# Kernel optimization log

Hardware: AMD Instinct MI355X
Metric: run time of the kernel (lower is better)

## Reference

```python
import jax, jax.numpy as jnp
import numpy as np

BUCKET_SIZE = 64  # must divide seq_len


def setup_inputs() -> dict:
    key = jax.random.key(0)
    k1, k2, k3, k4 = jax.random.split(key, 4)
    B, S, D = 4, 4096, 1024
    query = jax.random.normal(k1, (B, S, D), dtype=jnp.float32)
    key_t = jax.random.normal(k2, (B, S, D), dtype=jnp.float32)
    value = jax.random.normal(k3, (B, S, D), dtype=jnp.float32)
    # random hashing hyperplanes: [B, D, bucket_size // 2]
    R = jax.random.normal(k4, (B, D, BUCKET_SIZE // 2), dtype=jnp.float32)
    return {"query": query, "key": key_t, "value": value, "R": R}


def reference(query, key, value, R):
    B, S, D = query.shape
    # random projection: [B, S, bucket_size // 2]
    xR = jnp.einsum("bsd,bdr->bsr", query, R)
    # mirror trick -> [B, S, bucket_size]
    concat_xR = jnp.concatenate([xR, -xR], axis=-1)
    buckets = jnp.argmax(concat_xR, axis=-1)          # [B, S] int
    sticker = jnp.argsort(buckets, axis=-1)            # token permutation into buckets
    undo_sort = jnp.argsort(sticker, axis=-1)          # computed in original (unused)
    # batched gather (tf.gather batch_dims=1, axis=1)
    sorted_query = jnp.take_along_axis(query, sticker[..., None], axis=1)
    sorted_value = jnp.take_along_axis(value, sticker[..., None], axis=1)
    # tf.split(x, bucket_size, 1) then stack(axis=1) == reshape to chunks
    chunked_query = sorted_query.reshape(B, BUCKET_SIZE, S // BUCKET_SIZE, D)
    chunked_value = sorted_value.reshape(B, BUCKET_SIZE, S // BUCKET_SIZE, D)
    del undo_sort, chunked_query, chunked_value  # dead code in original; module returns sticker
    return sticker
```

## Files before the change

kernel.cpp:

```cpp
#include <hip/hip_runtime.h>


#define B_DIM 4
#define S_LEN 4096
#define D_DIM 1024
#define NR 32
#define NBK 64
#define TM 64
#define NCHUNK (S_LEN / TM)
#define NW 16
#define KSLICE (D_DIM / NW)

__global__ __launch_bounds__(1024, 4) void k1_buckets(
    const float* __restrict__ Q, const float* __restrict__ R,
    int* __restrict__ buckets, int* __restrict__ hist)
{
    __shared__ float buf[NW][NR][TM];
    __shared__ int cnt[NBK];

    const int t = threadIdx.x;
    const int b = blockIdx.x >> 6;
    const int chunk = blockIdx.x & 63;
    const int lane = t & 63;
    const int w = __builtin_amdgcn_readfirstlane(t >> 6);

    const int gtok = chunk * TM + lane;
    const float* Qrow = Q + ((size_t)b * S_LEN + gtok) * D_DIM + w * KSLICE;
    const float4* R4 = reinterpret_cast<const float4*>(
        R + (size_t)b * D_DIM * NR) + (size_t)w * KSLICE * (NR / 4);

    float4 acc[8];
#pragma unroll
    for (int rc = 0; rc < 8; ++rc) acc[rc] = make_float4(0.f, 0.f, 0.f, 0.f);

#pragma unroll
    for (int ph = 0; ph < 2; ++ph) {
        float4 qv[8];
#pragma unroll
        for (int j = 0; j < 8; ++j)
            qv[j] = *reinterpret_cast<const float4*>(Qrow + ph * 32 + j * 4);

#pragma unroll
        for (int kk = 0; kk < 32; ++kk) {
            const int k = ph * 32 + kk;
            const float4 qq = qv[kk >> 2];
            const float qk = ((kk & 3) == 0) ? qq.x
                           : ((kk & 3) == 1) ? qq.y
                           : ((kk & 3) == 2) ? qq.z : qq.w;
#pragma unroll
            for (int rc = 0; rc < 8; ++rc) {
                const float4 rv = R4[k * 8 + rc];
                acc[rc].x = fmaf(qk, rv.x, acc[rc].x);
                acc[rc].y = fmaf(qk, rv.y, acc[rc].y);
                acc[rc].z = fmaf(qk, rv.z, acc[rc].z);
                acc[rc].w = fmaf(qk, rv.w, acc[rc].w);
            }
        }
    }

#pragma unroll
    for (int rc = 0; rc < 8; ++rc) {
        buf[w][rc * 4 + 0][lane] = acc[rc].x;
        buf[w][rc * 4 + 1][lane] = acc[rc].y;
        buf[w][rc * 4 + 2][lane] = acc[rc].z;
        buf[w][rc * 4 + 3][lane] = acc[rc].w;
    }
    if (t < NBK) cnt[t] = 0;
    __syncthreads();

    if (t < TM) {
        float x[NR];
#pragma unroll
        for (int r = 0; r < NR; ++r) {
            float s = 0.f;
#pragma unroll
            for (int ww = 0; ww < NW; ++ww) s += buf[ww][r][t];
            x[r] = s;
        }
        float m1 = x[0]; int i1 = 0;
        float m2 = x[0]; int i2 = 0;
#pragma unroll
        for (int r = 1; r < NR; ++r) {
            const float v = x[r];
            if (v > m1) { m1 = v; i1 = r; }
            if (v < m2) { m2 = v; i2 = r; }
        }
        const int bk = (m1 >= -m2) ? i1 : (NR + i2);
        buckets[(size_t)b * S_LEN + chunk * TM + t] = bk;
        atomicAdd(&cnt[bk], 1);
    }
    __syncthreads();
    if (t < NBK) hist[((size_t)b * NCHUNK + chunk) * NBK + t] = cnt[t];
}

__global__ __launch_bounds__(256) void k2_scan(
    const int* __restrict__ hist, int* __restrict__ chunkOffset)
{
    const int t = threadIdx.x;
    const int b = t >> 6;
    const int bk = t & 63;
    const int lane = t & 63;

    int total = 0;
    for (int c = 0; c < NCHUNK; ++c)
        total += hist[((size_t)b * NCHUNK + c) * NBK + bk];

    int incl = total;
#pragma unroll
    for (int off = 1; off < 64; off <<= 1) {
        int n = __shfl_up(incl, off, 64);
        if (lane >= off) incl += n;
    }
    int run = incl - total;

    for (int c = 0; c < NCHUNK; ++c) {
        int h = hist[((size_t)b * NCHUNK + c) * NBK + bk];
        chunkOffset[((size_t)b * NCHUNK + c) * NBK + bk] = run;
        run += h;
    }
}

__global__ __launch_bounds__(256) void k3_scatter(
    const int* __restrict__ buckets, const int* __restrict__ chunkOffset,
    int* __restrict__ out)
{
    const int gid = blockIdx.x * 256 + threadIdx.x;
    const int b = gid >> 12;
    const int s = gid & (S_LEN - 1);
    const int chunk = s >> 6;
    const int lane = threadIdx.x & 63;

    const int bk = buckets[gid];

    unsigned long long m = ~0ull;
#pragma unroll
    for (int i = 0; i < 6; ++i) {
        unsigned long long bi = __ballot((bk >> i) & 1);
        m &= ((bk >> i) & 1) ? bi : ~bi;
    }
    int rank = __popcll(m & ((1ull << lane) - 1ull));

    int pos = chunkOffset[((size_t)b * NCHUNK + chunk) * NBK + bk] + rank;
    out[(size_t)b * S_LEN + pos] = s;
}

extern "C" void kernel_launch(void* const* d_in, const int* in_sizes, int n_in,
                              void* d_out, int out_size, void* d_ws, size_t ws_size,
                              hipStream_t stream) {
    const float* Q = (const float*)d_in[0];
    const float* R = (const float*)d_in[3];

    int* buckets     = (int*)d_ws;
    int* hist        = buckets + B_DIM * S_LEN;
    int* chunkOffset = hist + B_DIM * NCHUNK * NBK;

    k1_buckets<<<B_DIM * NCHUNK, 1024, 0, stream>>>(Q, R, buckets, hist);
    k2_scan   <<<1,              256,  0, stream>>>(hist, chunkOffset);
    k3_scatter<<<(B_DIM * S_LEN) / 256, 256, 0, stream>>>(buckets, chunkOffset, (int*)d_out);
}
```

Measured before the change: 46.17 us.

## Hold R slice in registers and stream Q tokens per wave with shuffle reduction

Rewrites the projection kernel so each lane keeps a 32-element column slice of R in registers. The wave then walks the 64 tokens of its chunk, loading each Q row segment as contiguous float4 vectors, double-buffered across token pairs. Partial dot products are combined with a cross-half shuffle and written to a padded shared buffer. The cross-wave reduction is now spread over all 1024 threads instead of 64. The aim is coalesced Q loads and the removal of repeated R global reads, at the cost of a serial per-token loop with more shared-memory stores and an extra barrier.

Measured after the change: 121.6 us. +163.3%, slower.

```diff
diff --git a/kernel.cpp b/kernel.cpp
--- a/kernel.cpp
+++ b/kernel.cpp
@@ -9,81 +9,90 @@
 #define TM 64
 #define NCHUNK (S_LEN / TM)
 #define NW 16
-#define KSLICE (D_DIM / NW)
+#define BUFP (NR + 1)
 
 __global__ __launch_bounds__(1024, 4) void k1_buckets(
     const float* __restrict__ Q, const float* __restrict__ R,
     int* __restrict__ buckets, int* __restrict__ hist)
 {
-    __shared__ float buf[NW][NR][TM];
+    __shared__ float buf[NW * TM * BUFP];
+    __shared__ float xs[NR * TM];
     __shared__ int cnt[NBK];
 
     const int t = threadIdx.x;
     const int b = blockIdx.x >> 6;
     const int chunk = blockIdx.x & 63;
+    const int w = t >> 6;
     const int lane = t & 63;
-    const int w = __builtin_amdgcn_readfirstlane(t >> 6);
+    const int r = lane & 31;
+    const int half = lane >> 5;
 
-    const int gtok = chunk * TM + lane;
-    const float* Qrow = Q + ((size_t)b * S_LEN + gtok) * D_DIM + w * KSLICE;
-    const float4* R4 = reinterpret_cast<const float4*>(
-        R + (size_t)b * D_DIM * NR) + (size_t)w * KSLICE * (NR / 4);
+    const float* Rb = R + (size_t)b * D_DIM * NR + (size_t)(w * 64 + half * 32) * NR + r;
+    float Rreg[32];
+#pragma unroll
+    for (int j = 0; j < 32; ++j) Rreg[j] = Rb[j * NR];
 
-    float4 acc[8];
+    const float* Qb = Q + ((size_t)b * S_LEN + chunk * TM) * D_DIM
+                    + w * 64 + half * 32;
+
+    float4 qA[8], qB[8];
 #pragma unroll
-    for (int rc = 0; rc < 8; ++rc) acc[rc] = make_float4(0.f, 0.f, 0.f, 0.f);
+    for (int i = 0; i < 8; ++i)
+        qA[i] = *reinterpret_cast<const float4*>(Qb + 0 * D_DIM + i * 4);
 
-#pragma unroll
-    for (int ph = 0; ph < 2; ++ph) {
-        float4 qv[8];
-#pragma unroll
-        for (int j = 0; j < 8; ++j)
-            qv[j] = *reinterpret_cast<const float4*>(Qrow + ph * 32 + j * 4);
-
-#pragma unroll
-        for (int kk = 0; kk < 32; ++kk) {
-            const int k = ph * 32 + kk;
-            const float4 qq = qv[kk >> 2];
-            const float qk = ((kk & 3) == 0) ? qq.x
-                           : ((kk & 3) == 1) ? qq.y
-                           : ((kk & 3) == 2) ? qq.z : qq.w;
-#pragma unroll
-            for (int rc = 0; rc < 8; ++rc) {
-                const float4 rv = R4[k * 8 + rc];
-                acc[rc].x = fmaf(qk, rv.x, acc[rc].x);
-                acc[rc].y = fmaf(qk, rv.y, acc[rc].y);
-                acc[rc].z = fmaf(qk, rv.z, acc[rc].z);
-                acc[rc].w = fmaf(qk, rv.w, acc[rc].w);
-            }
-        }
+#define COMPUTE(QV, TOK)                                                     \
+    {                                                                        \
+        float a0 = 0.f, a1 = 0.f, a2 = 0.f, a3 = 0.f;                        \
+        _Pragma("unroll")                                                    \
+        for (int i = 0; i < 8; ++i) {                                        \
+            a0 = fmaf(QV[i].x, Rreg[i * 4 + 0], a0);                         \
+            a1 = fmaf(QV[i].y, Rreg[i * 4 + 1], a1);                         \
+            a2 = fmaf(QV[i].z, Rreg[i * 4 + 2], a2);                         \
+            a3 = fmaf(QV[i].w, Rreg[i * 4 + 3], a3);                         \
+        }                                                                    \
+        float s = (a0 + a1) + (a2 + a3);                                     \
+        s += __shfl_xor(s, 32, 64);                                          \
+        buf[(w * TM + (TOK)) * BUFP + r] = s;                                \
     }
 
+    for (int tok = 0; tok < TM; tok += 2) {
 #pragma unroll
-    for (int rc = 0; rc < 8; ++rc) {
-        buf[w][rc * 4 + 0][lane] = acc[rc].x;
-        buf[w][rc * 4 + 1][lane] = acc[rc].y;
-        buf[w][rc * 4 + 2][lane] = acc[rc].z;
-        buf[w][rc * 4 + 3][lane] = acc[rc].w;
+        for (int i = 0; i < 8; ++i)
+            qB[i] = *reinterpret_cast<const float4*>(Qb + (size_t)(tok + 1) * D_DIM + i * 4);
+        COMPUTE(qA, tok)
+        if (tok + 2 < TM) {
+#pragma unroll
+            for (int i = 0; i < 8; ++i)
+                qA[i] = *reinterpret_cast<const float4*>(Qb + (size_t)(tok + 2) * D_DIM + i * 4);
+        }
+        COMPUTE(qB, tok + 1)
     }
+#undef COMPUTE
+
     if (t < NBK) cnt[t] = 0;
     __syncthreads();
 
+#pragma unroll
+    for (int it = 0; it < 2; ++it) {
+        const int p = t + it * 1024;
+        const int rr = p >> 6;
+        const int tk = p & 63;
+        float s = 0.f;
+#pragma unroll
+        for (int ww = 0; ww < NW; ++ww)
+            s += buf[(ww * TM + tk) * BUFP + rr];
+        xs[rr * TM + tk] = s;
+    }
+    __syncthreads();
+
     if (t < TM) {
-        float x[NR];
+        float m1 = xs[0 * TM + t]; int i1 = 0;
+        float m2 = m1;             int i2 = 0;
 #pragma unroll
-        for (int r = 0; r < NR; ++r) {
-            float s = 0.f;
-#pragma unroll
-            for (int ww = 0; ww < NW; ++ww) s += buf[ww][r][t];
-            x[r] = s;
-        }
-        float m1 = x[0]; int i1 = 0;
-        float m2 = x[0]; int i2 = 0;
-#pragma unroll
-        for (int r = 1; r < NR; ++r) {
-            const float v = x[r];
-            if (v > m1) { m1 = v; i1 = r; }
-            if (v < m2) { m2 = v; i2 = r; }
+        for (int rr = 1; rr < NR; ++rr) {
+            const float v = xs[rr * TM + t];
+            if (v > m1) { m1 = v; i1 = rr; }
+            if (v < m2) { m2 = v; i2 = rr; }
         }
         const int bk = (m1 >= -m2) ? i1 : (NR + i2);
         buckets[(size_t)b * S_LEN + chunk * TM + t] = bk;
```

## Stage Q and R tiles in swizzled LDS with 32-token chunks for projection

Applied to the files above, without the earlier changes.

The projection kernel now uses 32-token blocks of 512 threads. Each block stages 256-wide K tiles of Q (XOR-swizzled) and R into shared memory, and each thread computes an 8-token by 4-column register tile, where before each thread read R directly from global memory. Partial sums are reduced by a cross-half shuffle and then an LDS reduction across 8 waves. The histogram and scatter chunk size drops to 32, so the scan kernel walks twice as many chunks serially, and the scatter rank is computed per 32-lane half.

After: 44.88 us. 1.03x faster.

```diff
diff --git a/kernel.cpp b/kernel.cpp
--- a/kernel.cpp
+++ b/kernel.cpp
@@ -4,93 +4,136 @@
 #define B_DIM 4
 #define S_LEN 4096
 #define D_DIM 1024
-#define NR 32
+#define NRR 32
 #define NBK 64
-#define TM 64
-#define NCHUNK (S_LEN / TM)
-#define NW 16
-#define KSLICE (D_DIM / NW)
-
-__global__ __launch_bounds__(1024, 4) void k1_buckets(
-    const float* __restrict__ Q, const float* __restrict__ R,
-    int* __restrict__ buckets, int* __restrict__ hist)
+#define TMK 32
+#define NC32 (S_LEN / TMK)
+#define KB 256
+#define NTILE (D_DIM / KB)
+
+__global__ void __launch_bounds__(512) __attribute__((amdgpu_waves_per_eu(2, 4)))
+k1_buckets(const float* __restrict__ Q, const float* __restrict__ R,
+           int* __restrict__ buckets, int* __restrict__ hist)
 {
-    __shared__ float buf[NW][NR][TM];
+    __shared__ float lds[16384];
     __shared__ int cnt[NBK];
 
     const int t = threadIdx.x;
-    const int b = blockIdx.x >> 6;
-    const int chunk = blockIdx.x & 63;
+    const int b = blockIdx.x >> 7;
+    const int c32 = blockIdx.x & (NC32 - 1);
+
     const int lane = t & 63;
-    const int w = __builtin_amdgcn_readfirstlane(t >> 6);
-
-    const int gtok = chunk * TM + lane;
-    const float* Qrow = Q + ((size_t)b * S_LEN + gtok) * D_DIM + w * KSLICE;
-    const float4* R4 = reinterpret_cast<const float4*>(
-        R + (size_t)b * D_DIM * NR) + (size_t)w * KSLICE * (NR / 4);
+    const int w = t >> 6;
+    const int rq = lane & 7;
+    const int tg = (lane >> 3) & 3;
+    const int kh = lane >> 5;
+    const int kbase = w * 32 + kh * 16;
+
+    const float* Qg = Q + ((size_t)b * S_LEN + c32 * TMK) * D_DIM;
+    const float* Rg = R + (size_t)b * D_DIM * NRR;
 
     float4 acc[8];
 #pragma unroll
-    for (int rc = 0; rc < 8; ++rc) acc[rc] = make_float4(0.f, 0.f, 0.f, 0.f);
-
-#pragma unroll
-    for (int ph = 0; ph < 2; ++ph) {
-        float4 qv[8];
-#pragma unroll
-        for (int j = 0; j < 8; ++j)
-            qv[j] = *reinterpret_cast<const float4*>(Qrow + ph * 32 + j * 4);
-
-#pragma unroll
-        for (int kk = 0; kk < 32; ++kk) {
-            const int k = ph * 32 + kk;
-            const float4 qq = qv[kk >> 2];
-            const float qk = ((kk & 3) == 0) ? qq.x
-                           : ((kk & 3) == 1) ? qq.y
-                           : ((kk & 3) == 2) ? qq.z : qq.w;
-#pragma unroll
-            for (int rc = 0; rc < 8; ++rc) {
-                const float4 rv = R4[k * 8 + rc];
-                acc[rc].x = fmaf(qk, rv.x, acc[rc].x);
-                acc[rc].y = fmaf(qk, rv.y, acc[rc].y);
-                acc[rc].z = fmaf(qk, rv.z, acc[rc].z);
-                acc[rc].w = fmaf(qk, rv.w, acc[rc].w);
+    for (int j = 0; j < 8; ++j) acc[j] = make_float4(0.f, 0.f, 0.f, 0.f);
+
+    for (int tile = 0; tile < NTILE; ++tile) {
+        if (tile) __syncthreads();
+        {
+            const float* Qt = Qg + tile * KB;
+#pragma unroll
+            for (int i = 0; i < 4; ++i) {
+                const int f = t + 512 * i;
+                const int row = f >> 6;
+                const int q = f & 63;
+                const float4 v = *(const float4*)(Qt + (size_t)row * D_DIM + q * 4);
+                *(float4*)&lds[row * KB + ((q ^ (row >> 3)) << 2)] = v;
+            }
+            const float* Rt = Rg + (size_t)tile * KB * NRR;
+#pragma unroll
+            for (int i = 0; i < 4; ++i) {
+                const int f = t + 512 * i;
+                const float4 v = *(const float4*)(Rt + f * 4);
+                *(float4*)&lds[8192 + f * 4] = v;
             }
         }
-    }
-
-#pragma unroll
-    for (int rc = 0; rc < 8; ++rc) {
-        buf[w][rc * 4 + 0][lane] = acc[rc].x;
-        buf[w][rc * 4 + 1][lane] = acc[rc].y;
-        buf[w][rc * 4 + 2][lane] = acc[rc].z;
-        buf[w][rc * 4 + 3][lane] = acc[rc].w;
+        __syncthreads();
+#pragma unroll
+        for (int kk4 = 0; kk4 < 4; ++kk4) {
+            const int k0 = kbase + kk4 * 4;
+            const float4 rv0 = *(const float4*)&lds[8192 + (k0 + 0) * NRR + rq * 4];
+            const float4 rv1 = *(const float4*)&lds[8192 + (k0 + 1) * NRR + rq * 4];
+            const float4 rv2 = *(const float4*)&lds[8192 + (k0 + 2) * NRR + rq * 4];
+            const float4 rv3 = *(const float4*)&lds[8192 + (k0 + 3) * NRR + rq * 4];
+            const int qq = (k0 >> 2) ^ tg;
+#pragma unroll
+            for (int j = 0; j < 8; ++j) {
+                const int tok = tg * 8 + j;
+                const float4 q = *(const float4*)&lds[tok * KB + (qq << 2)];
+                acc[j].x = fmaf(q.x, rv0.x, acc[j].x);
+                acc[j].y = fmaf(q.x, rv0.y, acc[j].y);
+                acc[j].z = fmaf(q.x, rv0.z, acc[j].z);
+                acc[j].w = fmaf(q.x, rv0.w, acc[j].w);
+                acc[j].x = fmaf(q.y, rv1.x, acc[j].x);
+                acc[j].y = fmaf(q.y, rv1.y, acc[j].y);
+                acc[j].z = fmaf(q.y, rv1.z, acc[j].z);
+                acc[j].w = fmaf(q.y, rv1.w, acc[j].w);
+                acc[j].x = fmaf(q.z, rv2.x, acc[j].x);
+                acc[j].y = fmaf(q.z, rv2.y, acc[j].y);
+                acc[j].z = fmaf(q.z, rv2.z, acc[j].z);
+                acc[j].w = fmaf(q.z, rv2.w, acc[j].w);
+                acc[j].x = fmaf(q.w, rv3.x, acc[j].x);
+                acc[j].y = fmaf(q.w, rv3.y, acc[j].y);
+                acc[j].z = fmaf(q.w, rv3.z, acc[j].z);
+                acc[j].w = fmaf(q.w, rv3.w, acc[j].w);
+            }
+        }
+    }
+
+#pragma unroll
+    for (int j = 0; j < 8; ++j) {
+        acc[j].x += __shfl_xor(acc[j].x, 32, 64);
+        acc[j].y += __shfl_xor(acc[j].y, 32, 64);
+        acc[j].z += __shfl_xor(acc[j].z, 32, 64);
+        acc[j].w += __shfl_xor(acc[j].w, 32, 64);
     }
     if (t < NBK) cnt[t] = 0;
     __syncthreads();
 
-    if (t < TM) {
-        float x[NR];
-#pragma unroll
-        for (int r = 0; r < NR; ++r) {
-            float s = 0.f;
-#pragma unroll
-            for (int ww = 0; ww < NW; ++ww) s += buf[ww][r][t];
-            x[r] = s;
-        }
-        float m1 = x[0]; int i1 = 0;
-        float m2 = x[0]; int i2 = 0;
-#pragma unroll
-        for (int r = 1; r < NR; ++r) {
-            const float v = x[r];
+    if (kh == 0) {
+        float* red = &lds[8192 + w * (TMK * NRR)];
+#pragma unroll
+        for (int j = 0; j < 8; ++j)
+            *(float4*)&red[(tg * 8 + j) * NRR + rq * 4] = acc[j];
+    }
+    __syncthreads();
+
+#pragma unroll
+    for (int it = 0; it < 2; ++it) {
+        const int p = t + it * 512;
+        const int tok = p >> 5, r = p & 31;
+        float s = 0.f;
+#pragma unroll
+        for (int ww = 0; ww < 8; ++ww)
+            s += lds[8192 + ww * (TMK * NRR) + tok * NRR + r];
+        lds[tok * 33 + r] = s;
+    }
+    __syncthreads();
+
+    if (t < TMK) {
+        float m1 = lds[t * 33 + 0]; int i1 = 0;
+        float m2 = m1;              int i2 = 0;
+#pragma unroll
+        for (int r = 1; r < NRR; ++r) {
+            const float v = lds[t * 33 + r];
             if (v > m1) { m1 = v; i1 = r; }
             if (v < m2) { m2 = v; i2 = r; }
         }
-        const int bk = (m1 >= -m2) ? i1 : (NR + i2);
-        buckets[(size_t)b * S_LEN + chunk * TM + t] = bk;
+        const int bk = (m1 >= -m2) ? i1 : (NRR + i2);
+        buckets[(size_t)b * S_LEN + c32 * TMK + t] = bk;
         atomicAdd(&cnt[bk], 1);
     }
     __syncthreads();
-    if (t < NBK) hist[((size_t)b * NCHUNK + chunk) * NBK + t] = cnt[t];
+    if (t < NBK) hist[((size_t)b * NC32 + c32) * NBK + t] = cnt[t];
 }
 
 __global__ __launch_bounds__(256) void k2_scan(
@@ -102,8 +145,8 @@
     const int lane = t & 63;
 
     int total = 0;
-    for (int c = 0; c < NCHUNK; ++c)
-        total += hist[((size_t)b * NCHUNK + c) * NBK + bk];
+    for (int c = 0; c < NC32; ++c)
+        total += hist[((size_t)b * NC32 + c) * NBK + bk];
 
     int incl = total;
 #pragma unroll
@@ -113,9 +156,9 @@
     }
     int run = incl - total;
 
-    for (int c = 0; c < NCHUNK; ++c) {
-        int h = hist[((size_t)b * NCHUNK + c) * NBK + bk];
-        chunkOffset[((size_t)b * NCHUNK + c) * NBK + bk] = run;
+    for (int c = 0; c < NC32; ++c) {
+        int h = hist[((size_t)b * NC32 + c) * NBK + bk];
+        chunkOffset[((size_t)b * NC32 + c) * NBK + bk] = run;
         run += h;
     }
 }
@@ -127,7 +170,7 @@
     const int gid = blockIdx.x * 256 + threadIdx.x;
     const int b = gid >> 12;
     const int s = gid & (S_LEN - 1);
-    const int chunk = s >> 6;
+    const int chunk = s >> 5;
     const int lane = threadIdx.x & 63;
 
     const int bk = buckets[gid];
@@ -138,9 +181,10 @@
         unsigned long long bi = __ballot((bk >> i) & 1);
         m &= ((bk >> i) & 1) ? bi : ~bi;
     }
-    int rank = __popcll(m & ((1ull << lane) - 1ull));
-
-    int pos = chunkOffset[((size_t)b * NCHUNK + chunk) * NBK + bk] + rank;
+    const unsigned int m32 = (unsigned int)(m >> (lane & 32));
+    const int rank = __popc(m32 & ((1u << (lane & 31)) - 1u));
+
+    const int pos = chunkOffset[((size_t)b * NC32 + chunk) * NBK + bk] + rank;
     out[(size_t)b * S_LEN + pos] = s;
 }
 
@@ -152,9 +196,9 @@
 
     int* buckets     = (int*)d_ws;
     int* hist        = buckets + B_DIM * S_LEN;
-    int* chunkOffset = hist + B_DIM * NCHUNK * NBK;
-
-    k1_buckets<<<B_DIM * NCHUNK, 1024, 0, stream>>>(Q, R, buckets, hist);
-    k2_scan   <<<1,              256,  0, stream>>>(hist, chunkOffset);
+    int* chunkOffset = hist + B_DIM * NC32 * NBK;
+
+    k1_buckets<<<B_DIM * NC32, 512, 0, stream>>>(Q, R, buckets, hist);
+    k2_scan   <<<1,            256, 0, stream>>>(hist, chunkOffset);
     k3_scatter<<<(B_DIM * S_LEN) / 256, 256, 0, stream>>>(buckets, chunkOffset, (int*)d_out);
 }
```

## Restructure projection kernel with LDS-staged R and double-buffered Q tiles

Applied to the files above, without the earlier changes.

Rewrites the bucket projection kernel to use 256-thread blocks. R is staged into LDS with swizzled direct global-to-LDS loads, and Q tiles are streamed through double-buffered LDS using async loads overlapped with compute. Each thread now computes an 8-token by 8-hyperplane register tile, and the cross-lane reduction and argmax use shuffles instead of a shared-memory reduction buffer. The goal is more reuse of R, less redundant global traffic, and hidden load latency, at the cost of heavy LDS use (about 100KB) limiting occupancy to one block per CU and added complexity in the swizzle and waitcnt handling.

Measured after the change: 39.98 us. 13.4% less time.

```diff
diff --git a/kernel.cpp b/kernel.cpp
--- a/kernel.cpp
+++ b/kernel.cpp
@@ -4,90 +4,169 @@
 #define B_DIM 4
 #define S_LEN 4096
 #define D_DIM 1024
-#define NR 32
+#define NRR 32
 #define NBK 64
-#define TM 64
-#define NCHUNK (S_LEN / TM)
-#define NW 16
-#define KSLICE (D_DIM / NW)
-
-__global__ __launch_bounds__(1024, 4) void k1_buckets(
-    const float* __restrict__ Q, const float* __restrict__ R,
-    int* __restrict__ buckets, int* __restrict__ hist)
+#define TMK 64
+#define NCHUNK (S_LEN / TMK)
+#define QB 4096
+
+typedef const __attribute__((address_space(1))) void* gas_t;
+typedef __attribute__((address_space(3))) void* las_t;
+
+#define FMA4(A, S, B)                                                        \
+    (A).x = fmaf((S), (B).x, (A).x); (A).y = fmaf((S), (B).y, (A).y);        \
+    (A).z = fmaf((S), (B).z, (A).z); (A).w = fmaf((S), (B).w, (A).w);
+
+__global__ void __launch_bounds__(256) __attribute__((amdgpu_waves_per_eu(1, 1)))
+k1_buckets(const float* __restrict__ Q, const float* __restrict__ R,
+           int* __restrict__ buckets, int* __restrict__ hist)
 {
-    __shared__ float buf[NW][NR][TM];
+    __shared__ float4 smem4[QB + 2048];
     __shared__ int cnt[NBK];
 
     const int t = threadIdx.x;
     const int b = blockIdx.x >> 6;
     const int chunk = blockIdx.x & 63;
+
+    const int w = t >> 6;
     const int lane = t & 63;
-    const int w = __builtin_amdgcn_readfirstlane(t >> 6);
-
-    const int gtok = chunk * TM + lane;
-    const float* Qrow = Q + ((size_t)b * S_LEN + gtok) * D_DIM + w * KSLICE;
-    const float4* R4 = reinterpret_cast<const float4*>(
-        R + (size_t)b * D_DIM * NR) + (size_t)w * KSLICE * (NR / 4);
-
-    float4 acc[8];
-#pragma unroll
-    for (int rc = 0; rc < 8; ++rc) acc[rc] = make_float4(0.f, 0.f, 0.f, 0.f);
-
-#pragma unroll
-    for (int ph = 0; ph < 2; ++ph) {
-        float4 qv[8];
-#pragma unroll
-        for (int j = 0; j < 8; ++j)
-            qv[j] = *reinterpret_cast<const float4*>(Qrow + ph * 32 + j * 4);
-
-#pragma unroll
-        for (int kk = 0; kk < 32; ++kk) {
-            const int k = ph * 32 + kk;
-            const float4 qq = qv[kk >> 2];
-            const float qk = ((kk & 3) == 0) ? qq.x
-                           : ((kk & 3) == 1) ? qq.y
-                           : ((kk & 3) == 2) ? qq.z : qq.w;
-#pragma unroll
-            for (int rc = 0; rc < 8; ++rc) {
-                const float4 rv = R4[k * 8 + rc];
-                acc[rc].x = fmaf(qk, rv.x, acc[rc].x);
-                acc[rc].y = fmaf(qk, rv.y, acc[rc].y);
-                acc[rc].z = fmaf(qk, rv.z, acc[rc].z);
-                acc[rc].w = fmaf(qk, rv.w, acc[rc].w);
+    const int tok_t = lane >> 5;
+    const int r_t = (lane >> 3) & 3;
+    const int kl = lane & 7;
+
+    const float4* Qw4 = (const float4*)(Q + ((size_t)b * S_LEN + chunk * TMK + w * 16) * D_DIM);
+    const float4* Rg4 = (const float4*)(R + (size_t)b * D_DIM * NRR);
+
+#define STAGE_R(H)                                                            \
+    {                                                                         \
+        _Pragma("unroll")                                                     \
+        for (int i = 0; i < 16; ++i) {                                        \
+            const int rel = w * 1024 + i * 64 + lane;                         \
+            const int kh = rel >> 3, v = rel & 7;                             \
+            __builtin_amdgcn_global_load_lds(                                 \
+                (gas_t)(Rg4 + ((size_t)(H) * 512 + kh) * 8 + (v ^ ((kh >> 3) & 7))), \
+                (las_t)&smem4[w * 1024 + i * 64], 16, 0, 0);                  \
+        }                                                                     \
+    }
+
+#define ISSUE_Q(H, TILE, DST)                                                 \
+    {                                                                         \
+        _Pragma("unroll")                                                     \
+        for (int i = 0; i < 4; ++i) {                                         \
+            const int f = i * 64 + lane;                                      \
+            const int td = f >> 4, sd = f & 15;                               \
+            __builtin_amdgcn_global_load_lds(                                 \
+                (gas_t)(Qw4 + (size_t)td * 256 + (H) * 128 + (TILE) * 16      \
+                        + (sd ^ (td >> 3))),                                  \
+                (las_t)&smem4[QB + w * 512 + (DST) * 256 + i * 64], 16, 0, 0);\
+        }                                                                     \
+    }
+
+#define COMPUTE(TILE, BUF)                                                    \
+    {                                                                         \
+        const float4* qb = smem4 + QB + w * 512 + (BUF) * 256;                \
+        const float4* rb = smem4;                                             \
+        _Pragma("unroll")                                                     \
+        for (int kap = 0; kap < 2; ++kap) {                                   \
+            float4 qv[8];                                                     \
+            _Pragma("unroll")                                                 \
+            for (int j = 0; j < 8; ++j)                                       \
+                qv[j] = qb[(tok_t * 8 + j) * 16 + (((kl << 1) + kap) ^ tok_t)];\
+            _Pragma("unroll")                                                 \
+            for (int c = 0; c < 4; ++c) {                                     \
+                const int krow = (TILE) * 64 + kl * 8 + kap * 4 + c;          \
+                const float4 rv0 = rb[krow * 8 + ((r_t * 2 + 0) ^ kl)];       \
+                const float4 rv1 = rb[krow * 8 + ((r_t * 2 + 1) ^ kl)];       \
+                _Pragma("unroll")                                             \
+                for (int j = 0; j < 8; ++j) {                                 \
+                    const float s = c == 0 ? qv[j].x : c == 1 ? qv[j].y       \
+                                  : c == 2 ? qv[j].z : qv[j].w;               \
+                    FMA4(acc[j][0], s, rv0);                                  \
+                    FMA4(acc[j][1], s, rv1);                                  \
+                }                                                             \
+            }                                                                 \
+        }                                                                     \
+    }
+
+    float4 acc[8][2];
+#pragma unroll
+    for (int j = 0; j < 8; ++j) {
+        acc[j][0] = make_float4(0.f, 0.f, 0.f, 0.f);
+        acc[j][1] = make_float4(0.f, 0.f, 0.f, 0.f);
+    }
+    if (t < NBK) cnt[t] = 0;
+
+    for (int h = 0; h < 2; ++h) {
+        STAGE_R(h)
+        ISSUE_Q(h, 0, 0)
+        asm volatile("s_waitcnt vmcnt(0)" ::: "memory");
+        __syncthreads();
+
+        for (int tau = 0; tau < 8; ++tau) {
+            if (tau < 7) {
+                ISSUE_Q(h, tau + 1, (tau + 1) & 1)
+                asm volatile("s_waitcnt vmcnt(4)" ::: "memory");
+            } else {
+                asm volatile("s_waitcnt vmcnt(0)" ::: "memory");
             }
+            COMPUTE(tau, tau & 1)
         }
-    }
-
-#pragma unroll
-    for (int rc = 0; rc < 8; ++rc) {
-        buf[w][rc * 4 + 0][lane] = acc[rc].x;
-        buf[w][rc * 4 + 1][lane] = acc[rc].y;
-        buf[w][rc * 4 + 2][lane] = acc[rc].z;
-        buf[w][rc * 4 + 3][lane] = acc[rc].w;
-    }
-    if (t < NBK) cnt[t] = 0;
-    __syncthreads();
-
-    if (t < TM) {
-        float x[NR];
-#pragma unroll
-        for (int r = 0; r < NR; ++r) {
-            float s = 0.f;
-#pragma unroll
-            for (int ww = 0; ww < NW; ++ww) s += buf[ww][r][t];
-            x[r] = s;
+        __syncthreads();
+    }
+#undef STAGE_R
+#undef ISSUE_Q
+#undef COMPUTE
+
+#pragma unroll
+    for (int j = 0; j < 8; ++j)
+#pragma unroll
+        for (int p = 0; p < 2; ++p)
+#pragma unroll
+            for (int off = 1; off < 8; off <<= 1) {
+                acc[j][p].x += __shfl_xor(acc[j][p].x, off, 64);
+                acc[j][p].y += __shfl_xor(acc[j][p].y, off, 64);
+                acc[j][p].z += __shfl_xor(acc[j][p].z, off, 64);
+                acc[j][p].w += __shfl_xor(acc[j][p].w, off, 64);
+            }
+
+    int bkarr[8];
+#pragma unroll
+    for (int j = 0; j < 8; ++j) {
+        const int rbase = r_t * 8;
+        float m1 = acc[j][0].x; int i1 = rbase;
+        float m2 = m1;          int i2 = rbase;
+#pragma unroll
+        for (int p = 0; p < 2; ++p)
+#pragma unroll
+            for (int c = 0; c < 4; ++c) {
+                if (p == 0 && c == 0) continue;
+                const float v = p == 0
+                    ? (c == 1 ? acc[j][0].y : c == 2 ? acc[j][0].z : acc[j][0].w)
+                    : (c == 0 ? acc[j][1].x : c == 1 ? acc[j][1].y
+                              : c == 2 ? acc[j][1].z : acc[j][1].w);
+                const int r = rbase + p * 4 + c;
+                if (v > m1) { m1 = v; i1 = r; }
+                if (v < m2) { m2 = v; i2 = r; }
+            }
+#pragma unroll
+        for (int off = 8; off <= 16; off <<= 1) {
+            const float om1 = __shfl_xor(m1, off, 64);
+            const int   oi1 = __shfl_xor(i1, off, 64);
+            const float om2 = __shfl_xor(m2, off, 64);
+            const int   oi2 = __shfl_xor(i2, off, 64);
+            if (om1 > m1 || (om1 == m1 && oi1 < i1)) { m1 = om1; i1 = oi1; }
+            if (om2 < m2 || (om2 == m2 && oi2 < i2)) { m2 = om2; i2 = oi2; }
         }
-        float m1 = x[0]; int i1 = 0;
-        float m2 = x[0]; int i2 = 0;
-#pragma unroll
-        for (int r = 1; r < NR; ++r) {
-            const float v = x[r];
-            if (v > m1) { m1 = v; i1 = r; }
-            if (v < m2) { m2 = v; i2 = r; }
+        bkarr[j] = (m1 >= -m2) ? i1 : (NRR + i2);
+    }
+
+    if ((lane & 31) == 0) {
+#pragma unroll
+        for (int j = 0; j < 8; ++j) {
+            const int gtok = chunk * TMK + w * 16 + tok_t * 8 + j;
+            buckets[(size_t)b * S_LEN + gtok] = bkarr[j];
+            atomicAdd(&cnt[bkarr[j]], 1);
         }
-        const int bk = (m1 >= -m2) ? i1 : (NR + i2);
-        buckets[(size_t)b * S_LEN + chunk * TM + t] = bk;
-        atomicAdd(&cnt[bk], 1);
     }
     __syncthreads();
     if (t < NBK) hist[((size_t)b * NCHUNK + chunk) * NBK + t] = cnt[t];
@@ -154,7 +233,7 @@
     int* hist        = buckets + B_DIM * S_LEN;
     int* chunkOffset = hist + B_DIM * NCHUNK * NBK;
 
-    k1_buckets<<<B_DIM * NCHUNK, 1024, 0, stream>>>(Q, R, buckets, hist);
-    k2_scan   <<<1,              256,  0, stream>>>(hist, chunkOffset);
+    k1_buckets<<<B_DIM * NCHUNK, 256, 0, stream>>>(Q, R, buckets, hist);
+    k2_scan   <<<1,              256, 0, stream>>>(hist, chunkOffset);
     k3_scatter<<<(B_DIM * S_LEN) / 256, 256, 0, stream>>>(buckets, chunkOffset, (int*)d_out);
 }
```
